# Performance work log

Hardware: AMD Instinct MI355X
Metric: run time of the kernel (lower is better)

## Reference

```python
import jax, jax.numpy as jnp
import numpy as np

DIM_SIZE = 256
BASE_N = 10000.0


def setup_inputs() -> dict:
    key = jax.random.key(0)
    # timesteps / positions, uniform in [0, 1000)
    x = jax.random.uniform(key, (1048576,), dtype=jnp.float32) * 1000.0
    return {"x": x}


def reference(x) -> jnp.ndarray:
    half = DIM_SIZE // 2
    i = jnp.arange(half, dtype=x.dtype)            # [half]
    inv_freq = BASE_N ** (-2.0 * i / DIM_SIZE)     # [half]
    emb = x[:, None] * inv_freq[None, :]           # [N, half]
    # interleave: out[:, 2i] = sin(emb_i), out[:, 2i+1] = cos(emb_i)
    out = jnp.stack([jnp.sin(emb), jnp.cos(emb)], axis=-1)  # [N, half, 2]
    return out.reshape(x.shape[0], DIM_SIZE)
```

## Files before the change

### kernel.cpp

```cpp
#include <hip/hip_runtime.h>

#define DIM 256

__global__ __launch_bounds__(256) void SinusoidalEmbedding_kernel(
    const float* __restrict__ x, float* __restrict__ out, int n) {
    const int lane = threadIdx.x & 63;
    const int wid = blockIdx.x * (blockDim.x >> 6) + (threadIdx.x >> 6);
    const int nw = gridDim.x * (blockDim.x >> 6);

    const float k = 0.103810252965228506f;
    const float INV2PI = 0.15915494309189535f;
    const float i0 = (float)(2 * lane);
    const float g0 = exp2f(-i0 * k) * INV2PI;
    const float g1 = exp2f(-(i0 + 1.0f) * k) * INV2PI;

    for (int base = wid * 64; base < n; base += nw * 64) {
        const int nb = min(64, n - base);
        const float xv = (lane < nb) ? x[base + lane] : 0.0f;
        float* o = out + (size_t)base * DIM + lane * 4;

        if (nb == 64) {
            #pragma unroll 8
            for (int r = 0; r < 64; ++r) {
                const float xr = __shfl(xv, r);
                float t0 = xr * g0; t0 -= floorf(t0);
                float t1 = xr * g1; t1 -= floorf(t1);
                float4 v;
                v.x = __builtin_amdgcn_sinf(t0);
                v.y = __builtin_amdgcn_cosf(t0);
                v.z = __builtin_amdgcn_sinf(t1);
                v.w = __builtin_amdgcn_cosf(t1);
                *reinterpret_cast<float4*>(o + (size_t)r * DIM) = v;
            }
        } else {
            for (int r = 0; r < nb; ++r) {
                const float xr = __shfl(xv, r);
                float t0 = xr * g0; t0 -= floorf(t0);
                float t1 = xr * g1; t1 -= floorf(t1);
                float4 v;
                v.x = __builtin_amdgcn_sinf(t0);
                v.y = __builtin_amdgcn_cosf(t0);
                v.z = __builtin_amdgcn_sinf(t1);
                v.w = __builtin_amdgcn_cosf(t1);
                *reinterpret_cast<float4*>(o + (size_t)r * DIM) = v;
            }
        }
    }
}

extern "C" void kernel_launch(void* const* d_in, const int* in_sizes, int n_in,
                              void* d_out, int out_size, void* d_ws, size_t ws_size,
                              hipStream_t stream) {
    const float* x = (const float*)d_in[0];
    float* out = (float*)d_out;
    const int n = in_sizes[0];

    const int block = 256;
    const int grid = 2048;
    SinusoidalEmbedding_kernel<<<grid, block, 0, stream>>>(x, out, n);
}
```

Measured before the change: 193.7 us.

## Interleave row assignment across waves so concurrent stores hit adjacent rows

Rows are now assigned to waves with a grid-stride pattern, so wave w handles rows w, w+nw, w+2nw and so on, instead of each wave owning a contiguous block of 64 rows. At any moment all waves write neighbouring rows, which is meant to make the write stream more sequential across the device and improve DRAM page locality. Each iteration processes 128 rows from two strided gathers of x. The x loads become uncoalesced strided gathers, and the tail handling becomes more complex.

```diff
diff --git a/kernel.cpp b/kernel.cpp
--- a/kernel.cpp
+++ b/kernel.cpp
@@ -10,19 +10,23 @@
 
     const float k = 0.103810252965228506f;
     const float INV2PI = 0.15915494309189535f;
-    const float i0 = (float)(2 * lane);
-    const float g0 = exp2f(-i0 * k) * INV2PI;
-    const float g1 = exp2f(-(i0 + 1.0f) * k) * INV2PI;
+    const float i0f = (float)(2 * lane);
+    const float g0 = exp2f(-i0f * k) * INV2PI;
+    const float g1 = exp2f(-(i0f + 1.0f) * k) * INV2PI;
 
-    for (int base = wid * 64; base < n; base += nw * 64) {
-        const int nb = min(64, n - base);
-        const float xv = (lane < nb) ? x[base + lane] : 0.0f;
-        float* o = out + (size_t)base * DIM + lane * 4;
+    for (long ib = 0; wid + ib * (long)nw < n; ib += 128) {
+        const long rg0 = wid + (ib + lane) * (long)nw;
+        const long rg1 = wid + (ib + 64 + lane) * (long)nw;
+        const float xg0 = (rg0 < n) ? x[rg0] : 0.0f;
+        const float xg1 = (rg1 < n) ? x[rg1] : 0.0f;
+        const bool full = (wid + (ib + 127) * (long)nw) < n;
 
-        if (nb == 64) {
+        if (full) {
+            float* o = out + (size_t)(wid + ib * (size_t)nw) * DIM + lane * 4;
+            const size_t stride = (size_t)nw * DIM;
             #pragma unroll 8
-            for (int r = 0; r < 64; ++r) {
-                const float xr = __shfl(xv, r);
+            for (int i = 0; i < 64; ++i) {
+                const float xr = __shfl(xg0, i);
                 float t0 = xr * g0; t0 -= floorf(t0);
                 float t1 = xr * g1; t1 -= floorf(t1);
                 float4 v;
@@ -30,11 +34,12 @@
                 v.y = __builtin_amdgcn_cosf(t0);
                 v.z = __builtin_amdgcn_sinf(t1);
                 v.w = __builtin_amdgcn_cosf(t1);
-                *reinterpret_cast<float4*>(o + (size_t)r * DIM) = v;
+                *reinterpret_cast<float4*>(o + (size_t)i * stride) = v;
             }
-        } else {
-            for (int r = 0; r < nb; ++r) {
-                const float xr = __shfl(xv, r);
+            float* o2 = o + 64 * stride;
+            #pragma unroll 8
+            for (int i = 0; i < 64; ++i) {
+                const float xr = __shfl(xg1, i);
                 float t0 = xr * g0; t0 -= floorf(t0);
                 float t1 = xr * g1; t1 -= floorf(t1);
                 float4 v;
@@ -42,7 +47,21 @@
                 v.y = __builtin_amdgcn_cosf(t0);
                 v.z = __builtin_amdgcn_sinf(t1);
                 v.w = __builtin_amdgcn_cosf(t1);
-                *reinterpret_cast<float4*>(o + (size_t)r * DIM) = v;
+                *reinterpret_cast<float4*>(o2 + (size_t)i * stride) = v;
+            }
+        } else {
+            for (int i = 0; i < 128; ++i) {
+                const long row = wid + (ib + i) * (long)nw;
+                if (row >= n) break;
+                const float xr = (i < 64) ? __shfl(xg0, i & 63) : __shfl(xg1, i & 63);
+                float t0 = xr * g0; t0 -= floorf(t0);
+                float t1 = xr * g1; t1 -= floorf(t1);
+                float4 v;
+                v.x = __builtin_amdgcn_sinf(t0);
+                v.y = __builtin_amdgcn_cosf(t0);
+                v.z = __builtin_amdgcn_sinf(t1);
+                v.w = __builtin_amdgcn_cosf(t1);
+                *reinterpret_cast<float4*>(out + (size_t)row * DIM + lane * 4) = v;
             }
         }
     }
```

New measurement: 224.5 us. 1.16x slower.

## Assign contiguous row blocks per wave, fully unroll, use fract builtin, shrink grid

Applied to the files above, without the earlier changes.

Each wave now handles a contiguous range of 64-row blocks instead of striding across the grid, and the tail rows go to a single wave. The inner loop is fully unrolled and uses the hardware fract instruction in place of subtracting floor. The grid shrinks from 2048 to 256 blocks, giving 1024 waves that each write longer contiguous output spans. The kernel is bound by output writes (1 GiB); fewer resident waves may reduce memory-level parallelism and lower achievable write bandwidth.

```diff
diff --git a/kernel.cpp b/kernel.cpp
--- a/kernel.cpp
+++ b/kernel.cpp
@@ -10,40 +10,48 @@
 
     const float k = 0.103810252965228506f;
     const float INV2PI = 0.15915494309189535f;
-    const float i0 = (float)(2 * lane);
-    const float g0 = exp2f(-i0 * k) * INV2PI;
-    const float g1 = exp2f(-(i0 + 1.0f) * k) * INV2PI;
+    const float i0f = (float)(2 * lane);
+    const float g0 = exp2f(-i0f * k) * INV2PI;
+    const float g1 = exp2f(-(i0f + 1.0f) * k) * INV2PI;
 
-    for (int base = wid * 64; base < n; base += nw * 64) {
-        const int nb = min(64, n - base);
-        const float xv = (lane < nb) ? x[base + lane] : 0.0f;
+    const int B = n >> 6;
+    const int K = B / nw;
+    const int R = B % nw;
+    const int myK = K + (wid < R ? 1 : 0);
+    const int first = wid * K + (wid < R ? wid : R);
+
+    for (int b = 0; b < myK; ++b) {
+        const int base = (first + b) << 6;
+        const float xv = x[base + lane];
         float* o = out + (size_t)base * DIM + lane * 4;
+        #pragma unroll
+        for (int r = 0; r < 64; ++r) {
+            const float xr = __shfl(xv, r);
+            const float t0 = __builtin_amdgcn_fractf(xr * g0);
+            const float t1 = __builtin_amdgcn_fractf(xr * g1);
+            float4 v;
+            v.x = __builtin_amdgcn_sinf(t0);
+            v.y = __builtin_amdgcn_cosf(t0);
+            v.z = __builtin_amdgcn_sinf(t1);
+            v.w = __builtin_amdgcn_cosf(t1);
+            *reinterpret_cast<float4*>(o + (size_t)r * DIM) = v;
+        }
+    }
 
-        if (nb == 64) {
-            #pragma unroll 8
-            for (int r = 0; r < 64; ++r) {
-                const float xr = __shfl(xv, r);
-                float t0 = xr * g0; t0 -= floorf(t0);
-                float t1 = xr * g1; t1 -= floorf(t1);
-                float4 v;
-                v.x = __builtin_amdgcn_sinf(t0);
-                v.y = __builtin_amdgcn_cosf(t0);
-                v.z = __builtin_amdgcn_sinf(t1);
-                v.w = __builtin_amdgcn_cosf(t1);
-                *reinterpret_cast<float4*>(o + (size_t)r * DIM) = v;
-            }
-        } else {
-            for (int r = 0; r < nb; ++r) {
-                const float xr = __shfl(xv, r);
-                float t0 = xr * g0; t0 -= floorf(t0);
-                float t1 = xr * g1; t1 -= floorf(t1);
-                float4 v;
-                v.x = __builtin_amdgcn_sinf(t0);
-                v.y = __builtin_amdgcn_cosf(t0);
-                v.z = __builtin_amdgcn_sinf(t1);
-                v.w = __builtin_amdgcn_cosf(t1);
-                *reinterpret_cast<float4*>(o + (size_t)r * DIM) = v;
-            }
+    const int tail = n & 63;
+    if (tail && wid == 0) {
+        const int base = B << 6;
+        const float xv = (lane < tail) ? x[base + lane] : 0.0f;
+        for (int r = 0; r < tail; ++r) {
+            const float xr = __shfl(xv, r);
+            const float t0 = __builtin_amdgcn_fractf(xr * g0);
+            const float t1 = __builtin_amdgcn_fractf(xr * g1);
+            float4 v;
+            v.x = __builtin_amdgcn_sinf(t0);
+            v.y = __builtin_amdgcn_cosf(t0);
+            v.z = __builtin_amdgcn_sinf(t1);
+            v.w = __builtin_amdgcn_cosf(t1);
+            *reinterpret_cast<float4*>(out + (size_t)(base + r) * DIM + lane * 4) = v;
         }
     }
 }
@@ -56,6 +64,6 @@
     const int n = in_sizes[0];
 
     const int block = 256;
-    const int grid = 2048;
+    const int grid = 256;
     SinusoidalEmbedding_kernel<<<grid, block, 0, stream>>>(x, out, n);
 }
```

After: 204.7 us. 5.7% more time.
